# Performance work log

Measured on AMD Instinct MI355X. Metric: run time of the kernel, lower is better.

## Reference

```python
import jax, jax.numpy as jnp
import numpy as np

E, R, D = 500000, 1000, 128      # entity_num, relation_num, dim
B, KN, KP, KE = 8192, 64, 64, 16  # batch of nodes; padded context sizes


def setup_inputs() -> dict:
    key = jax.random.key(0)
    ks = jax.random.split(key, 13)
    ids = lambda k, s: jax.random.randint(k, s, 0, E)
    flg = lambda k, s: jax.random.randint(k, s, 0, 2).astype(bool)
    return {
        "ent_emb": jax.random.normal(ks[0], (E, D), jnp.float32) * 0.02,
        "rel_emb": jax.random.normal(ks[1], (R, D), jnp.float32) * 0.02,
        "node_ids": ids(ks[2], (B,)),
        "node_is_rel": flg(ks[3], (B,)),
        "nbr_ids": ids(ks[4], (B, KN)),
        "nbr_is_rel": flg(ks[5], (B, KN)),
        "nbr_mask": flg(ks[6], (B, KN)),
        "path_ids": ids(ks[7], (B, KP)),
        "path_is_rel": flg(ks[8], (B, KP)),
        "path_mask": flg(ks[9], (B, KP)),
        "edge_ids": ids(ks[10], (B, KE)),
        "edge_is_rel": flg(ks[11], (B, KE)),
        "edge_mask": flg(ks[12], (B, KE)),
    }


def _lookup(ent_emb, rel_emb, node_ids, is_rel):
    # mirrors get_embedding: relation nodes use rel table, else entity table
    return jnp.where(is_rel[..., None], rel_emb[node_ids % R], ent_emb[node_ids])


def _log_p(si_emb, ctx_emb, ctx_mask, accumulate):
    # C = [si; context], shape [B, 1+K, D]; row 0 (si) always valid
    C = jnp.concatenate([si_emb[:, None, :], ctx_emb], axis=1)
    m = jnp.concatenate([jnp.ones((C.shape[0], 1), bool), ctx_mask], axis=1)
    Cm = jnp.where(m[..., None], C, 0.0)
    # context_pie = sum(C, 0) / ||C||_F  (torch.norm over full tensor)
    pie = Cm.sum(axis=1) / jnp.sqrt((Cm * Cm).sum(axis=(1, 2)))[:, None]
    scores = jnp.einsum('bkd,bd->bk', C, pie)
    logp = jax.nn.log_softmax(jnp.where(m, scores, -jnp.inf), axis=1)
    if accumulate:
        return jnp.where(m, logp, 0.0).sum(axis=1)
    return logp[:, 0]


def reference(ent_emb, rel_emb, node_ids, node_is_rel,
              nbr_ids, nbr_is_rel, nbr_mask,
              path_ids, path_is_rel, path_mask,
              edge_ids, edge_is_rel, edge_mask):
    si = _lookup(ent_emb, rel_emb, node_ids, node_is_rel)          # [B, D]
    ln = _log_p(si, _lookup(ent_emb, rel_emb, nbr_ids, nbr_is_rel), nbr_mask, True)
    lp = _log_p(si, _lookup(ent_emb, rel_emb, path_ids, path_is_rel), path_mask, True)
    le = _log_p(si, _lookup(ent_emb, rel_emb, edge_ids, edge_is_rel), edge_mask, False)
    # loss = -(1*neighbors + 0.1*paths + 0.1*edges) per node
    return -(ln + 0.1 * lp + 0.1 * le)
```

## Files before the change

kernel.cpp:

```cpp
#include <hip/hip_runtime.h>
#include <math.h>
#include <stdint.h>


constexpr int E_ = 500000;
constexpr int R_ = 1000;
constexpr int D_ = 128;
constexpr int KN_ = 64, KP_ = 64, KE_ = 16;
constexpr int ROWW = 65;
constexpr int NROWS = 65;

struct Smem {
  uint32_t c[NROWS * ROWW];
  alignas(16) float S[D_];
  alignas(16) float Spart[2][D_];
  float red[8];
  int cmeta[64];
  int Vsh;
};

__device__ __forceinline__ float wadd(float v) {
#pragma unroll
  for (int off = 32; off > 0; off >>= 1) v += __shfl_down(v, off, 64);
  return v;
}
__device__ __forceinline__ float wmax(float v) {
#pragma unroll
  for (int off = 32; off > 0; off >>= 1) v = fmaxf(v, __shfl_down(v, off, 64));
  return v;
}
__device__ __forceinline__ uint32_t f2bf(float v) {
  const uint32_t u = __float_as_uint(v);
  return (u + 0x7fffu + ((u >> 16) & 1u)) >> 16;
}

template <int K, bool ACC>
__device__ float ctx_logp(Smem& sm, float si_d, float sqsi,
                          const float* __restrict__ ent,
                          const float* __restrict__ rel,
                          const int* __restrict__ ids,
                          const int* __restrict__ isrel,
                          const int* __restrict__ mask) {
  const int d = threadIdx.x;
  const int w = d >> 6;
  const int lane = d & 63;
  const int g = lane >> 5;
  const int cq = lane & 31;

  __syncthreads();

  if (w == 0) {
    int m = 0, midx = 0;
    if (lane < K) {
      m = mask[lane];
      const int id = ids[lane];
      midx = isrel[lane] ? E_ + (id % R_) : id;
    }
    const unsigned long long bal = __ballot(m != 0);
    const int pos = __popcll(bal & ((1ull << lane) - 1ull));
    if (m) sm.cmeta[pos] = midx;
    if (lane == 0) sm.Vsh = (int)__popcll(bal);
  }
  __syncthreads();
  const int V = sm.Vsh;

  const int half = (V + 1) >> 1;
  const int rs = w * half;
  const int re = (V < rs + half) ? V : (rs + half);
  float4 Sp = make_float4(0.f, 0.f, 0.f, 0.f);
  float sq = 0.f;
#pragma unroll 8
  for (int r2 = rs; r2 < re; r2 += 2) {
    const int r = r2 + g;
    const bool on = (r < re);
    const int midx = sm.cmeta[on ? r : rs];
    const float* base = (midx >= E_) ? rel + (size_t)(midx - E_) * D_
                                     : ent + (size_t)midx * D_;
    float4 v = *(const float4*)(base + 4 * cq);
    if (!on) { v.x = 0.f; v.y = 0.f; v.z = 0.f; v.w = 0.f; }
    Sp.x += v.x; Sp.y += v.y; Sp.z += v.z; Sp.w += v.w;
    sq += v.x * v.x + v.y * v.y + v.z * v.z + v.w * v.w;
    if (on) {
      uint32_t* rw = sm.c + (size_t)(r + 1) * ROWW;
      rw[2 * cq] = f2bf(v.x) | (f2bf(v.y) << 16);
      rw[2 * cq + 1] = f2bf(v.z) | (f2bf(v.w) << 16);
    }
  }
  Sp.x += __shfl_xor(Sp.x, 32, 64);
  Sp.y += __shfl_xor(Sp.y, 32, 64);
  Sp.z += __shfl_xor(Sp.z, 32, 64);
  Sp.w += __shfl_xor(Sp.w, 32, 64);
  if (lane < 32) *(float4*)&sm.Spart[w][4 * cq] = Sp;
  const float wq = wadd(sq);
  if (lane == 0) sm.red[w] = wq;
  __syncthreads();

  sm.S[d] = si_d + sm.Spart[0][d] + sm.Spart[1][d];
  const float invn = rsqrtf(sqsi + sm.red[0] + sm.red[1]);
  __syncthreads();

  float score = 0.f;
  const bool valid = (d <= V);
  if (valid) {
    const uint32_t* row = sm.c + (size_t)d * ROWW;
    const float2* S2 = (const float2*)sm.S;
    float acc = 0.f;
#pragma unroll
    for (int jj = 0; jj < D_ / 2; ++jj) {
      const uint32_t t = row[jj];
      const float2 s2 = S2[jj];
      acc += __uint_as_float(t << 16) * s2.x;
      acc += __uint_as_float(t & 0xffff0000u) * s2.y;
    }
    score = acc * invn;
  }

  const float wm = wmax(valid ? score : -INFINITY);
  if (lane == 0) sm.red[2 + w] = wm;
  __syncthreads();
  const float mx = fmaxf(sm.red[2], sm.red[3]);

  const float we = wadd(valid ? __expf(score - mx) : 0.f);
  const float ws = wadd(valid ? score : 0.f);
  if (lane == 0) { sm.red[4 + w] = we; sm.red[6 + w] = ws; }
  __syncthreads();
  const float logZ = __logf(sm.red[4] + sm.red[5]);
  if (ACC) {
    return (sm.red[6] + sm.red[7]) - (float)(V + 1) * (mx + logZ);
  } else {
    return score - mx - logZ;
  }
}

__global__ __launch_bounds__(128, 4) void gake_kernel(
    const float* __restrict__ ent, const float* __restrict__ rel,
    const int* __restrict__ node_ids, const int* __restrict__ node_isrel,
    const int* __restrict__ nbr_ids, const int* __restrict__ nbr_isrel,
    const int* __restrict__ nbr_mask, const int* __restrict__ path_ids,
    const int* __restrict__ path_isrel, const int* __restrict__ path_mask,
    const int* __restrict__ edge_ids, const int* __restrict__ edge_isrel,
    const int* __restrict__ edge_mask, float* __restrict__ out) {
  __shared__ Smem sm;
  const int b = blockIdx.x;
  const int d = threadIdx.x;
  const int w = d >> 6;
  const int lane = d & 63;

  const int nid = node_ids[b];
  const float* srow = node_isrel[b] ? rel + (size_t)(nid % R_) * D_
                                    : ent + (size_t)nid * D_;
  const float si_d = srow[d];
  ((uint16_t*)sm.c)[d] = (uint16_t)f2bf(si_d);

  const float wq = wadd(si_d * si_d);
  if (lane == 0) sm.red[w] = wq;
  __syncthreads();
  const float sqsi = sm.red[0] + sm.red[1];

  const float ln = ctx_logp<KN_, true>(sm, si_d, sqsi, ent, rel,
                                       nbr_ids + (size_t)b * KN_,
                                       nbr_isrel + (size_t)b * KN_,
                                       nbr_mask + (size_t)b * KN_);
  const float lp = ctx_logp<KP_, true>(sm, si_d, sqsi, ent, rel,
                                       path_ids + (size_t)b * KP_,
                                       path_isrel + (size_t)b * KP_,
                                       path_mask + (size_t)b * KP_);
  const float le = ctx_logp<KE_, false>(sm, si_d, sqsi, ent, rel,
                                        edge_ids + (size_t)b * KE_,
                                        edge_isrel + (size_t)b * KE_,
                                        edge_mask + (size_t)b * KE_);
  if (d == 0) out[b] = -(ln + 0.1f * lp + 0.1f * le);
}

extern "C" void kernel_launch(void* const* d_in, const int* in_sizes, int n_in,
                              void* d_out, int out_size, void* d_ws,
                              size_t ws_size, hipStream_t stream) {
  const float* ent = (const float*)d_in[0];
  const float* rel = (const float*)d_in[1];
  const int* node_ids = (const int*)d_in[2];
  const int* node_isrel = (const int*)d_in[3];
  const int* nbr_ids = (const int*)d_in[4];
  const int* nbr_isrel = (const int*)d_in[5];
  const int* nbr_mask = (const int*)d_in[6];
  const int* path_ids = (const int*)d_in[7];
  const int* path_isrel = (const int*)d_in[8];
  const int* path_mask = (const int*)d_in[9];
  const int* edge_ids = (const int*)d_in[10];
  const int* edge_isrel = (const int*)d_in[11];
  const int* edge_mask = (const int*)d_in[12];
  float* out = (float*)d_out;

  const int B = in_sizes[2];
  gake_kernel<<<B, 128, 0, stream>>>(
      ent, rel, node_ids, node_isrel, nbr_ids, nbr_isrel, nbr_mask, path_ids,
      path_isrel, path_mask, edge_ids, edge_isrel, edge_mask, out);
}
```

Baseline: 400.9 us.

## Split contexts across blocks and compute softmax terms from register-held rows

The kernel now launches three blocks per node, one per context type, and combines the results with atomicAdd into a zeroed output. Gathered rows stay in registers instead of a bf16 shared-memory matrix. The summed-score term is computed algebraically from |S|^2 and si·S, and the log-softmax uses an online max/sum over wave-reduced dot products. This removes the large shared-memory buffer and the serial per-row dot loop, which should raise occupancy and parallelism. The cost is an extra memset, atomics, three reloads of the si row, and float-order nondeterminism in the output.

```diff
diff --git a/kernel.cpp b/kernel.cpp
--- a/kernel.cpp
+++ b/kernel.cpp
@@ -6,36 +6,23 @@
 constexpr int E_ = 500000;
 constexpr int R_ = 1000;
 constexpr int D_ = 128;
-constexpr int KN_ = 64, KP_ = 64, KE_ = 16;
-constexpr int ROWW = 65;
-constexpr int NROWS = 65;
 
 struct Smem {
-  uint32_t c[NROWS * ROWW];
-  alignas(16) float S[D_];
-  alignas(16) float Spart[2][D_];
+  alignas(16) float si[D_];
+  alignas(16) float Sp[2][D_];
   float red[8];
   int cmeta[64];
   int Vsh;
 };
 
-__device__ __forceinline__ float wadd(float v) {
-#pragma unroll
-  for (int off = 32; off > 0; off >>= 1) v += __shfl_down(v, off, 64);
+__device__ __forceinline__ float bsum(float v) {
+#pragma unroll
+  for (int off = 1; off < 64; off <<= 1) v += __shfl_xor(v, off, 64);
   return v;
 }
-__device__ __forceinline__ float wmax(float v) {
-#pragma unroll
-  for (int off = 32; off > 0; off >>= 1) v = fmaxf(v, __shfl_down(v, off, 64));
-  return v;
-}
-__device__ __forceinline__ uint32_t f2bf(float v) {
-  const uint32_t u = __float_as_uint(v);
-  return (u + 0x7fffu + ((u >> 16) & 1u)) >> 16;
-}
 
 template <int K, bool ACC>
-__device__ float ctx_logp(Smem& sm, float si_d, float sqsi,
+__device__ float ctx_term(Smem& sm, float si_d,
                           const float* __restrict__ ent,
                           const float* __restrict__ rel,
                           const int* __restrict__ ids,
@@ -46,8 +33,7 @@
   const int lane = d & 63;
   const int g = lane >> 5;
   const int cq = lane & 31;
-
-  __syncthreads();
+  constexpr int MAXIT = (K / 2 + 1) / 2;
 
   if (w == 0) {
     int m = 0, midx = 0;
@@ -57,79 +43,96 @@
       midx = isrel[lane] ? E_ + (id % R_) : id;
     }
     const unsigned long long bal = __ballot(m != 0);
-    const int pos = __popcll(bal & ((1ull << lane) - 1ull));
-    if (m) sm.cmeta[pos] = midx;
+    if (m) sm.cmeta[__popcll(bal & ((1ull << lane) - 1ull))] = midx;
     if (lane == 0) sm.Vsh = (int)__popcll(bal);
   }
   __syncthreads();
   const int V = sm.Vsh;
-
   const int half = (V + 1) >> 1;
   const int rs = w * half;
-  const int re = (V < rs + half) ? V : (rs + half);
-  float4 Sp = make_float4(0.f, 0.f, 0.f, 0.f);
-  float sq = 0.f;
-#pragma unroll 8
-  for (int r2 = rs; r2 < re; r2 += 2) {
-    const int r = r2 + g;
-    const bool on = (r < re);
-    const int midx = sm.cmeta[on ? r : rs];
+  const int re = min(V, rs + half);
+
+  float4 stash[MAXIT];
+#pragma unroll
+  for (int it = 0; it < MAXIT; ++it) {
+    const int r = rs + 2 * it + g;
+    if (rs + 2 * it >= re) break;
+    int midx = 0;
+    if (r < re) midx = sm.cmeta[r];
     const float* base = (midx >= E_) ? rel + (size_t)(midx - E_) * D_
                                      : ent + (size_t)midx * D_;
     float4 v = *(const float4*)(base + 4 * cq);
-    if (!on) { v.x = 0.f; v.y = 0.f; v.z = 0.f; v.w = 0.f; }
+    if (r >= re) { v.x = 0.f; v.y = 0.f; v.z = 0.f; v.w = 0.f; }
+    stash[it] = v;
+  }
+
+  float4 Sp = make_float4(0.f, 0.f, 0.f, 0.f);
+  float sq = si_d * si_d;
+#pragma unroll
+  for (int it = 0; it < MAXIT; ++it) {
+    if (rs + 2 * it >= re) break;
+    const float4 v = stash[it];
     Sp.x += v.x; Sp.y += v.y; Sp.z += v.z; Sp.w += v.w;
     sq += v.x * v.x + v.y * v.y + v.z * v.z + v.w * v.w;
-    if (on) {
-      uint32_t* rw = sm.c + (size_t)(r + 1) * ROWW;
-      rw[2 * cq] = f2bf(v.x) | (f2bf(v.y) << 16);
-      rw[2 * cq + 1] = f2bf(v.z) | (f2bf(v.w) << 16);
-    }
   }
   Sp.x += __shfl_xor(Sp.x, 32, 64);
   Sp.y += __shfl_xor(Sp.y, 32, 64);
   Sp.z += __shfl_xor(Sp.z, 32, 64);
   Sp.w += __shfl_xor(Sp.w, 32, 64);
-  if (lane < 32) *(float4*)&sm.Spart[w][4 * cq] = Sp;
-  const float wq = wadd(sq);
+  if (lane < 32) *(float4*)&sm.Sp[w][4 * cq] = Sp;
+  const float wq = bsum(sq);
   if (lane == 0) sm.red[w] = wq;
   __syncthreads();
 
-  sm.S[d] = si_d + sm.Spart[0][d] + sm.Spart[1][d];
-  const float invn = rsqrtf(sqsi + sm.red[0] + sm.red[1]);
+  const float4 si4 = *(const float4*)&sm.si[4 * cq];
+  const float4 a0 = *(const float4*)&sm.Sp[0][4 * cq];
+  const float4 a1 = *(const float4*)&sm.Sp[1][4 * cq];
+  float4 S4;
+  S4.x = si4.x + a0.x + a1.x;
+  S4.y = si4.y + a0.y + a1.y;
+  S4.z = si4.z + a0.z + a1.z;
+  S4.w = si4.w + a0.w + a1.w;
+  const float invn = rsqrtf(sm.red[0] + sm.red[1]);
+
+  const float t1 = S4.x * S4.x + S4.y * S4.y + S4.z * S4.z + S4.w * S4.w;
+  const float t2 = si4.x * S4.x + si4.y * S4.y + si4.z * S4.z + si4.w * S4.w;
+  const float sum_s = bsum(t1) * 0.5f * invn;
+  const float s0 = bsum(t2) * 0.5f * invn;
+
+  float m = -INFINITY, l = 0.f;
+#pragma unroll
+  for (int it = 0; it < MAXIT; ++it) {
+    if (rs + 2 * it >= re) break;
+    const int r = rs + 2 * it + g;
+    const float4 v = stash[it];
+    float p = v.x * S4.x + v.y * S4.y + v.z * S4.z + v.w * S4.w;
+#pragma unroll
+    for (int off = 1; off < 32; off <<= 1) p += __shfl_xor(p, off, 64);
+    if (r < re) {
+      const float s = p * invn;
+      const float mn = fmaxf(m, s);
+      l = l * __expf(m - mn) + __expf(s - mn);
+      m = mn;
+    }
+  }
+  const float m2 = __shfl_xor(m, 32, 64);
+  const float l2 = __shfl_xor(l, 32, 64);
+  const float mw = fmaxf(m, m2);
+  const float lw = (mw == -INFINITY)
+                       ? 0.f
+                       : l * __expf(m - mw) + l2 * __expf(m2 - mw);
+  if (lane == 0) { sm.red[2 + w] = mw; sm.red[4 + w] = lw; }
   __syncthreads();
 
-  float score = 0.f;
-  const bool valid = (d <= V);
-  if (valid) {
-    const uint32_t* row = sm.c + (size_t)d * ROWW;
-    const float2* S2 = (const float2*)sm.S;
-    float acc = 0.f;
-#pragma unroll
-    for (int jj = 0; jj < D_ / 2; ++jj) {
-      const uint32_t t = row[jj];
-      const float2 s2 = S2[jj];
-      acc += __uint_as_float(t << 16) * s2.x;
-      acc += __uint_as_float(t & 0xffff0000u) * s2.y;
-    }
-    score = acc * invn;
-  }
-
-  const float wm = wmax(valid ? score : -INFINITY);
-  if (lane == 0) sm.red[2 + w] = wm;
-  __syncthreads();
-  const float mx = fmaxf(sm.red[2], sm.red[3]);
-
-  const float we = wadd(valid ? __expf(score - mx) : 0.f);
-  const float ws = wadd(valid ? score : 0.f);
-  if (lane == 0) { sm.red[4 + w] = we; sm.red[6 + w] = ws; }
-  __syncthreads();
-  const float logZ = __logf(sm.red[4] + sm.red[5]);
-  if (ACC) {
-    return (sm.red[6] + sm.red[7]) - (float)(V + 1) * (mx + logZ);
-  } else {
-    return score - mx - logZ;
-  }
+  const float m0 = sm.red[2], m1 = sm.red[3];
+  const float l0 = sm.red[4], l1 = sm.red[5];
+  const float mfin = fmaxf(fmaxf(m0, m1), s0);
+  const float lfin = l0 * __expf(m0 - mfin) + l1 * __expf(m1 - mfin) +
+                     __expf(s0 - mfin);
+  const float logZ = __logf(lfin);
+
+  if (ACC) return sum_s - (float)(V + 1) * (mfin + logZ);
+  return s0 - mfin - logZ;
 }
 
 __global__ __launch_bounds__(128, 4) void gake_kernel(
@@ -139,37 +142,37 @@
     const int* __restrict__ nbr_mask, const int* __restrict__ path_ids,
     const int* __restrict__ path_isrel, const int* __restrict__ path_mask,
     const int* __restrict__ edge_ids, const int* __restrict__ edge_isrel,
-    const int* __restrict__ edge_mask, float* __restrict__ out) {
+    const int* __restrict__ edge_mask, float* __restrict__ out, int B) {
   __shared__ Smem sm;
-  const int b = blockIdx.x;
+  const int bid = blockIdx.x;
+  const int ctx = bid / B;
+  const int b = bid - ctx * B;
   const int d = threadIdx.x;
-  const int w = d >> 6;
-  const int lane = d & 63;
 
   const int nid = node_ids[b];
   const float* srow = node_isrel[b] ? rel + (size_t)(nid % R_) * D_
                                     : ent + (size_t)nid * D_;
   const float si_d = srow[d];
-  ((uint16_t*)sm.c)[d] = (uint16_t)f2bf(si_d);
-
-  const float wq = wadd(si_d * si_d);
-  if (lane == 0) sm.red[w] = wq;
-  __syncthreads();
-  const float sqsi = sm.red[0] + sm.red[1];
-
-  const float ln = ctx_logp<KN_, true>(sm, si_d, sqsi, ent, rel,
-                                       nbr_ids + (size_t)b * KN_,
-                                       nbr_isrel + (size_t)b * KN_,
-                                       nbr_mask + (size_t)b * KN_);
-  const float lp = ctx_logp<KP_, true>(sm, si_d, sqsi, ent, rel,
-                                       path_ids + (size_t)b * KP_,
-                                       path_isrel + (size_t)b * KP_,
-                                       path_mask + (size_t)b * KP_);
-  const float le = ctx_logp<KE_, false>(sm, si_d, sqsi, ent, rel,
-                                        edge_ids + (size_t)b * KE_,
-                                        edge_isrel + (size_t)b * KE_,
-                                        edge_mask + (size_t)b * KE_);
-  if (d == 0) out[b] = -(ln + 0.1f * lp + 0.1f * le);
+  sm.si[d] = si_d;
+
+  float term, wgt;
+  if (ctx == 0) {
+    term = ctx_term<64, true>(sm, si_d, ent, rel, nbr_ids + (size_t)b * 64,
+                              nbr_isrel + (size_t)b * 64,
+                              nbr_mask + (size_t)b * 64);
+    wgt = 1.0f;
+  } else if (ctx == 1) {
+    term = ctx_term<64, true>(sm, si_d, ent, rel, path_ids + (size_t)b * 64,
+                              path_isrel + (size_t)b * 64,
+                              path_mask + (size_t)b * 64);
+    wgt = 0.1f;
+  } else {
+    term = ctx_term<16, false>(sm, si_d, ent, rel, edge_ids + (size_t)b * 16,
+                               edge_isrel + (size_t)b * 16,
+                               edge_mask + (size_t)b * 16);
+    wgt = 0.1f;
+  }
+  if (d == 0) atomicAdd(out + b, -wgt * term);
 }
 
 extern "C" void kernel_launch(void* const* d_in, const int* in_sizes, int n_in,
@@ -191,7 +194,8 @@
   float* out = (float*)d_out;
 
   const int B = in_sizes[2];
-  gake_kernel<<<B, 128, 0, stream>>>(
+  hipMemsetAsync(d_out, 0, (size_t)out_size * sizeof(float), stream);
+  gake_kernel<<<3 * B, 128, 0, stream>>>(
       ent, rel, node_ids, node_isrel, nbr_ids, nbr_isrel, nbr_mask, path_ids,
-      path_isrel, path_mask, edge_ids, edge_isrel, edge_mask, out);
-}
+      path_isrel, path_mask, edge_ids, edge_isrel, edge_mask, out, B);
+}
```

New measurement: 404.4 us. No clear change (+0.9%).
